# Performance work log

Measured on AMD Instinct MI355X. Metric: run time of the kernel, lower is better.

## Reference

```python
import jax, jax.numpy as jnp
import numpy as np

NEG_SLOPE = 0.2  # PyG GATConv default leaky_relu slope


def _gat_layer(x, src, dst, W, a_src, a_dst, b, N, concat):
    # x: [N, F_in]; W: [F_in, H*C]; a_src/a_dst: [H, C]; b: [H*C] or [C]
    H, C = a_src.shape
    h = (x @ W).reshape(N, H, C)                      # [N, H, C]
    al_s = jnp.einsum('nhc,hc->nh', h, a_src)          # [N, H]
    al_d = jnp.einsum('nhc,hc->nh', h, a_dst)          # [N, H]
    e = jax.nn.leaky_relu(al_s[src] + al_d[dst], NEG_SLOPE)  # [E, H]
    # segment softmax over incoming edges of each dst node
    m = jax.ops.segment_max(e, dst, num_segments=N)    # [N, H]
    ex = jnp.exp(e - m[dst])                           # [E, H]
    denom = jax.ops.segment_sum(ex, dst, num_segments=N)
    attn = ex / denom[dst]                             # [E, H]
    msg = (h[src] * attn[:, :, None]).reshape(-1, H * C)  # [E, H*C]
    out = jax.ops.segment_sum(msg, dst, num_segments=N)   # [N, H*C]
    if concat:
        return out + b
    return out.reshape(N, H, C).mean(axis=1) + b


def setup_inputs() -> dict:
    key = jax.random.key(0)
    ks = jax.random.split(key, 20)
    N, E, D, C, H = 20000, 160000, 768, 128, 4
    HC = H * C  # 512
    def glorot(k, shape):
        fan = shape[0] + shape[-1]
        return jax.random.uniform(k, shape, jnp.float32, -1.0, 1.0) * np.sqrt(6.0 / fan)
    inp = {
        'x': jax.random.normal(ks[0], (N, D), jnp.float32),
        'edge_index': jax.random.randint(ks[1], (2, E), 0, N, jnp.int64),
        'W1': glorot(ks[2], (D, HC)),  'as1': glorot(ks[3], (H, C)), 'ad1': glorot(ks[4], (H, C)), 'b1': jnp.zeros((HC,), jnp.float32),
        'W2': glorot(ks[5], (HC, HC)), 'as2': glorot(ks[6], (H, C)), 'ad2': glorot(ks[7], (H, C)), 'b2': jnp.zeros((HC,), jnp.float32),
        'W3': glorot(ks[8], (HC, C)),  'as3': glorot(ks[9], (1, C)), 'ad3': glorot(ks[10], (1, C)), 'b3': jnp.zeros((C,), jnp.float32),
        'Ws1': glorot(ks[11], (C, C // 2)), 'bs1': jnp.zeros((C // 2,), jnp.float32),
        'Ws2': glorot(ks[12], (C // 2, 1)), 'bs2': jnp.zeros((1,), jnp.float32),
    }
    return inp


def reference(x, edge_index, W1, as1, ad1, b1, W2, as2, ad2, b2, W3, as3, ad3, b3, Ws1, bs1, Ws2, bs2):
    N = x.shape[0]
    loops = jnp.arange(N, dtype=edge_index.dtype)
    src = jnp.concatenate([edge_index[0], loops])  # add self-loops (PyG default)
    dst = jnp.concatenate([edge_index[1], loops])
    h = _gat_layer(x, src, dst, W1, as1, ad1, b1, N, concat=True)
    h = jax.nn.relu(h)  # dropout is identity in eval mode
    h = _gat_layer(h, src, dst, W2, as2, ad2, b2, N, concat=True)
    h = jax.nn.relu(h)
    h = _gat_layer(h, src, dst, W3, as3, ad3, b3, N, concat=False)
    # risk scoring head: Linear -> ReLU -> Linear -> Sigmoid
    s = jax.nn.relu(h @ Ws1 + bs1)
    return jax.nn.sigmoid(s @ Ws2 + bs2)  # [N, 1]
```

## Files before the change

### kernel.cpp

```cpp
#include <hip/hip_runtime.h>
#include <hip/hip_bf16.h>
#include <math.h>

#define NEG_SLOPE 0.2f
#define MAXDEG 64

typedef __attribute__((ext_vector_type(8))) __bf16 bf16x8;
typedef __attribute__((ext_vector_type(4))) float f32x4;

__device__ inline float lrelu(float v) { return v > 0.f ? v : NEG_SLOPE * v; }

__device__ inline unsigned short f2bf(float f) {
    __hip_bfloat16 h = __float2bfloat16(f);
    return *reinterpret_cast<unsigned short*>(&h);
}
__device__ inline float bf_lo(unsigned u) { return __uint_as_float(u << 16); }
__device__ inline float bf_hi(unsigned u) { return __uint_as_float(u & 0xffff0000u); }

__device__ inline void gld16(const unsigned short* gp, unsigned short* lp) {
    __builtin_amdgcn_global_load_lds(
        (const __attribute__((address_space(1))) void*)gp,
        (__attribute__((address_space(3))) void*)lp, 16, 0, 0);
}

__device__ inline void transpose_one(const float* __restrict__ in,
                                     unsigned short* __restrict__ out,
                                     int K, int N, int idx) {
    if (idx >= K * N) return;
    int n = idx / K, k = idx % K;
    out[(size_t)n * K + k] = f2bf(in[(size_t)k * N + n]);
}

#define BARRIER()    asm volatile("s_barrier" ::: "memory")
#define WAIT_LGKM0() asm volatile("s_waitcnt lgkmcnt(0)" ::: "memory")
#define WAIT_VM0()   asm volatile("s_waitcnt vmcnt(0)" ::: "memory")
#define WAIT_VM3()   asm volatile("s_waitcnt vmcnt(3)" ::: "memory")
#define WAIT_VM6()   asm volatile("s_waitcnt vmcnt(6)" ::: "memory")

__global__ __launch_bounds__(256) void preproc_kernel(
    const float* __restrict__ x, unsigned short* __restrict__ xbf, int n4,
    const float* __restrict__ W1, unsigned short* __restrict__ W1t,
    const float* __restrict__ W2, unsigned short* __restrict__ W2t,
    const float* __restrict__ W3, unsigned short* __restrict__ W3t,
    const float* __restrict__ Ws1, unsigned short* __restrict__ Ws1t,
    const int* __restrict__ ei, int E, int N,
    int* __restrict__ cursor, int* __restrict__ csr,
    int c0, int c1, int c2, int c3, int c4,
    int D, int HC, int C) {
    int b = blockIdx.x;
    int t = threadIdx.x;
    if (b < c0) {
        int i = b * 256 + t;
        if (i < n4) {
            float4 v = reinterpret_cast<const float4*>(x)[i];
            ushort4 o;
            o.x = f2bf(v.x); o.y = f2bf(v.y); o.z = f2bf(v.z); o.w = f2bf(v.w);
            reinterpret_cast<ushort4*>(xbf)[i] = o;
        }
        return;
    }
    b -= c0;
    if (b < c1) { transpose_one(W1, W1t, D, HC, b * 256 + t); return; }
    b -= c1;
    if (b < c2) { transpose_one(W2, W2t, HC, HC, b * 256 + t); return; }
    b -= c2;
    if (b < c3) { transpose_one(W3, W3t, HC, C, b * 256 + t); return; }
    b -= c3;
    if (b < c4) { transpose_one(Ws1, Ws1t, 128, 64, b * 256 + t); return; }
    b -= c4;
    {
        int e = b * 256 + t;
        if (e < E + N) {
            int src, dst;
            if (e < E) { src = ei[e]; dst = ei[E + e]; }
            else       { src = dst = e - E; }
            int pos = atomicAdd(&cursor[dst], 1);
            if (pos < MAXDEG) csr[dst * MAXDEG + pos] = src;
        }
    }
}

template <int HEADS>
__global__ __launch_bounds__(512) void gemm_big(const unsigned short* __restrict__ A,
                                                const unsigned short* __restrict__ Bt,
                                                unsigned short* __restrict__ Cc,
                                                int M, int N, int K, int rowTiles,
                                                const float* __restrict__ a_src,
                                                const float* __restrict__ a_dst,
                                                float* __restrict__ alS,
                                                float* __restrict__ alD) {
    __shared__ unsigned short Asl[3][128 * 32];
    __shared__ unsigned short Bsl[3][256 * 32];
    const int tid  = threadIdx.x;
    const int lane = tid & 63;
    const int wave = tid >> 6;

    int r, c;
    {
        int b = blockIdx.x;
        int mainRows = rowTiles & ~7;
        int mainBlocks = mainRows * 2;
        if (b < mainBlocks) {
            int xcd = b & 7;
            c = (b >> 3) & 1;
            r = (b >> 4) * 8 + xcd;
        } else {
            int idx = b - mainBlocks;
            r = mainRows + (idx >> 1);
            c = idx & 1;
        }
    }
    const int rowBase = r * 128;
    const int colBase = c * 256;
    const int wm = (wave & 1) * 64;
    const int wn = (wave >> 1) * 64;
    const int q   = lane >> 4;
    const int l16 = lane & 15;

    const int ar  = tid >> 2;
    const int acg = (tid & 3) ^ ((ar >> 1) & 3);
    int gaA = rowBase + ar; if (gaA >= M) gaA = M - 1;
    const unsigned short* gpA0 = A + (size_t)gaA * K + acg * 8;

    const int br0  = tid >> 2;
    const int bcg0 = (tid & 3) ^ ((br0 >> 1) & 3);
    const int br1  = (tid + 512) >> 2;
    const int bcg1 = (tid & 3) ^ ((br1 >> 1) & 3);
    const unsigned short* gpB0 = Bt + (size_t)(colBase + br0) * K + bcg0 * 8;
    const unsigned short* gpB1 = Bt + (size_t)(colBase + br1) * K + bcg1 * 8;

    const int nk = K >> 5;
    f32x4 acc[4][4] = {};

    auto stage = [&](int kt, int buf) {
        gld16(gpA0 + kt * 32, &Asl[buf][tid * 8]);
        gld16(gpB0 + kt * 32, &Bsl[buf][tid * 8]);
        gld16(gpB1 + kt * 32, &Bsl[buf][(size_t)(tid + 512) * 8]);
    };
    auto compute = [&](int buf) {
        bf16x8 af[4], bfv[4];
#pragma unroll
        for (int mi = 0; mi < 4; mi++) {
            int row = wm + mi * 16 + l16;
            int ch = q ^ ((row >> 1) & 3);
            af[mi] = *reinterpret_cast<const bf16x8*>(&Asl[buf][row * 32 + ch * 8]);
        }
#pragma unroll
        for (int ni = 0; ni < 4; ni++) {
            int row = wn + ni * 16 + l16;
            int ch = q ^ ((row >> 1) & 3);
            bfv[ni] = *reinterpret_cast<const bf16x8*>(&Bsl[buf][row * 32 + ch * 8]);
        }
#pragma unroll
        for (int mi = 0; mi < 4; mi++)
#pragma unroll
            for (int ni = 0; ni < 4; ni++)
                acc[mi][ni] = __builtin_amdgcn_mfma_f32_16x16x32_bf16(af[mi], bfv[ni], acc[mi][ni], 0, 0, 0);
    };

    stage(0, 0);
    stage(1, 1);
    int buf = 0;
    for (int kt = 0; kt < nk; kt++) {
        if (kt + 2 < nk) {
            int nbuf = buf + 2; if (nbuf >= 3) nbuf -= 3;
            stage(kt + 2, nbuf);
            WAIT_VM6();
        } else if (kt + 1 < nk) {
            WAIT_VM3();
        } else {
            WAIT_VM0();
        }
        BARRIER();
        compute(buf);
        WAIT_LGKM0();
        BARRIER();
        buf++; if (buf >= 3) buf = 0;
    }

    const int headBase = colBase >> 7;
    const int hl   = wn >> 7;
    const int half = (wn >> 6) & 1;
    const float* aslp = a_src + (headBase + hl) * 128;
    const float* adlp = a_dst + (headBase + hl) * 128;
    float acoef[4], dcoef[4];
#pragma unroll
    for (int ni = 0; ni < 4; ni++) {
        int cl = half * 64 + ni * 16 + l16;
        acoef[ni] = aslp[cl];
        dcoef[ni] = adlp[cl];
    }

    float2* red = reinterpret_cast<float2*>(&Asl[0][0]);

#pragma unroll
    for (int mi = 0; mi < 4; mi++) {
#pragma unroll
        for (int rr = 0; rr < 4; rr++) {
            int lrow = wm + mi * 16 + q * 4 + rr;
            int grow = rowBase + lrow;
            bool ok = grow < M;
            float vs = 0.f, vd = 0.f;
#pragma unroll
            for (int ni = 0; ni < 4; ni++) {
                float hv = acc[mi][ni][rr];
                vs += hv * acoef[ni];
                vd += hv * dcoef[ni];
                if (ok) {
                    int gcol = colBase + wn + ni * 16 + l16;
                    Cc[(size_t)grow * N + gcol] = f2bf(hv);
                }
            }
#pragma unroll
            for (int d = 1; d < 16; d <<= 1) {
                vs += __shfl_xor(vs, d);
                vd += __shfl_xor(vd, d);
            }
            if (l16 == 0) red[lrow * 4 + hl * 2 + half] = make_float2(vs, vd);
        }
    }
    __syncthreads();
    if (tid < 256) {
        int row = tid >> 1, hh = tid & 1;
        int grow = rowBase + row;
        if (grow < M) {
            float2 a = red[row * 4 + hh * 2 + 0];
            float2 b = red[row * 4 + hh * 2 + 1];
            alS[(size_t)grow * HEADS + headBase + hh] = a.x + b.x;
            alD[(size_t)grow * HEADS + headBase + hh] = a.y + b.y;
        }
    }
}

__global__ __launch_bounds__(256) void gemm_l3(const unsigned short* __restrict__ A,
                                               const unsigned short* __restrict__ Bt,
                                               unsigned short* __restrict__ Cc,
                                               int M, int K,
                                               const float* __restrict__ a_src,
                                               const float* __restrict__ a_dst,
                                               float* __restrict__ alS,
                                               float* __restrict__ alD) {
    const int N = 128;
    __shared__ unsigned short Asl[3][64 * 32];
    __shared__ unsigned short Bsl[3][128 * 32];
    const int tid  = threadIdx.x;
    const int lane = tid & 63;
    const int wave = tid >> 6;
    const int rowBase = blockIdx.x * 64;
    const int wm = (wave & 1) * 32;
    const int wn = (wave >> 1) * 64;
    const int q   = lane >> 4;
    const int l16 = lane & 15;

    const int ar  = tid >> 2;
    const int acg = (tid & 3) ^ ((ar >> 1) & 3);
    int gaA = rowBase + ar; if (gaA >= M) gaA = M - 1;
    const unsigned short* gpA0 = A + (size_t)gaA * K + acg * 8;

    const int br0  = tid >> 2;
    const int bcg0 = (tid & 3) ^ ((br0 >> 1) & 3);
    const int br1  = (tid + 256) >> 2;
    const int bcg1 = (tid & 3) ^ ((br1 >> 1) & 3);
    const unsigned short* gpB0 = Bt + (size_t)br0 * K + bcg0 * 8;
    const unsigned short* gpB1 = Bt + (size_t)br1 * K + bcg1 * 8;

    const int nk = K >> 5;
    f32x4 acc[2][4] = {};

    auto stage = [&](int kt, int buf) {
        gld16(gpA0 + kt * 32, &Asl[buf][tid * 8]);
        gld16(gpB0 + kt * 32, &Bsl[buf][tid * 8]);
        gld16(gpB1 + kt * 32, &Bsl[buf][(size_t)(tid + 256) * 8]);
    };
    auto compute = [&](int buf) {
        bf16x8 af[2], bfv[4];
#pragma unroll
        for (int mi = 0; mi < 2; mi++) {
            int row = wm + mi * 16 + l16;
            int ch = q ^ ((row >> 1) & 3);
            af[mi] = *reinterpret_cast<const bf16x8*>(&Asl[buf][row * 32 + ch * 8]);
        }
#pragma unroll
        for (int ni = 0; ni < 4; ni++) {
            int row = wn + ni * 16 + l16;
            int ch = q ^ ((row >> 1) & 3);
            bfv[ni] = *reinterpret_cast<const bf16x8*>(&Bsl[buf][row * 32 + ch * 8]);
        }
#pragma unroll
        for (int mi = 0; mi < 2; mi++)
#pragma unroll
            for (int ni = 0; ni < 4; ni++)
                acc[mi][ni] = __builtin_amdgcn_mfma_f32_16x16x32_bf16(af[mi], bfv[ni], acc[mi][ni], 0, 0, 0);
    };

    stage(0, 0);
    stage(1, 1);
    int buf = 0;
    for (int kt = 0; kt < nk; kt++) {
        if (kt + 2 < nk) {
            int nbuf = buf + 2; if (nbuf >= 3) nbuf -= 3;
            stage(kt + 2, nbuf);
            WAIT_VM6();
        } else if (kt + 1 < nk) {
            WAIT_VM3();
        } else {
            WAIT_VM0();
        }
        BARRIER();
        compute(buf);
        WAIT_LGKM0();
        BARRIER();
        buf++; if (buf >= 3) buf = 0;
    }

    const int half = wn >> 6;
    float acoef[4], dcoef[4];
#pragma unroll
    for (int ni = 0; ni < 4; ni++) {
        int cl = wn + ni * 16 + l16;
        acoef[ni] = a_src[cl];
        dcoef[ni] = a_dst[cl];
    }

    float2* red = reinterpret_cast<float2*>(&Asl[0][0]);

#pragma unroll
    for (int mi = 0; mi < 2; mi++) {
#pragma unroll
        for (int rr = 0; rr < 4; rr++) {
            int lrow = wm + mi * 16 + q * 4 + rr;
            int grow = rowBase + lrow;
            bool ok = grow < M;
            float vs = 0.f, vd = 0.f;
#pragma unroll
            for (int ni = 0; ni < 4; ni++) {
                float hv = acc[mi][ni][rr];
                vs += hv * acoef[ni];
                vd += hv * dcoef[ni];
                if (ok) {
                    int gcol = wn + ni * 16 + l16;
                    Cc[(size_t)grow * N + gcol] = f2bf(hv);
                }
            }
#pragma unroll
            for (int d = 1; d < 16; d <<= 1) {
                vs += __shfl_xor(vs, d);
                vd += __shfl_xor(vd, d);
            }
            if (l16 == 0) red[lrow * 2 + half] = make_float2(vs, vd);
        }
    }
    __syncthreads();
    if (tid < 64) {
        int grow = rowBase + tid;
        if (grow < M) {
            float2 a = red[tid * 2 + 0];
            float2 b = red[tid * 2 + 1];
            alS[grow] = a.x + b.x;
            alD[grow] = a.y + b.y;
        }
    }
}

template <int H, int C, int MODE>
__global__ __launch_bounds__(256) void gat_aggregate(const unsigned short* __restrict__ hb,
                                                     const float* __restrict__ alS,
                                                     const float* __restrict__ alD,
                                                     const int* __restrict__ cursor,
                                                     const int* __restrict__ csr_src,
                                                     const float* __restrict__ bias,
                                                     unsigned short* __restrict__ outbuf,
                                                     int N,
                                                     const unsigned short* __restrict__ Ws1t,
                                                     const float* __restrict__ bs1,
                                                     const float* __restrict__ Ws2,
                                                     const float* __restrict__ bs2,
                                                     float* __restrict__ out) {
    constexpr int HC = H * C;
    constexpr int PER = HC / 64;
    __shared__ float hrow[4][128];

    int n = (blockIdx.x * blockDim.x + threadIdx.x) >> 6;
    int lane = threadIdx.x & 63;
    int wave = threadIdx.x >> 6;
    if (n >= N) return;
    const int* rowp = csr_src + (size_t)n * MAXDEG;

    const int grp  = lane >> 4;
    const int slot = lane & 15;
    const int gbase = lane & 48;
    const int myh  = (H == 4) ? grp : 0;
    const unsigned short* hbl = hb + (size_t)lane * PER;

    int total = cursor[n];
    const float adh = alD[n * H + myh];
    if (total > MAXDEG) total = MAXDEG;

    float m = -1e30f, dn = 0.f;
    float acc0 = 0.f, acc1 = 0.f, acc2 = 0.f, acc3 = 0.f,
          acc4 = 0.f, acc5 = 0.f, acc6 = 0.f, acc7 = 0.f;

    for (int base = 0; base < total; base += 16) {
        int cnt = total - base; if (cnt > 16) cnt = 16;
        int cntR = (cnt + 3) & ~3;
        bool act = slot < cnt;

        int s_raw = rowp[base + slot];
        int s_safe = ((unsigned)s_raw < (unsigned)N) ? s_raw : 0;
        float av = alS[(size_t)s_safe * H + myh];

        uint4 g0 = {}, g1 = {}, g2 = {}, g3 = {};
        uint4 g4 = {}, g5 = {}, g6 = {}, g7 = {};
        uint4 g8 = {}, g9 = {}, g10 = {}, g11 = {};
        uint4 g12 = {}, g13 = {}, g14 = {}, g15 = {};
        unsigned h0 = 0, h1 = 0, h2 = 0, h3 = 0;
        unsigned h4 = 0, h5 = 0, h6 = 0, h7 = 0;
        unsigned h8 = 0, h9 = 0, h10 = 0, h11 = 0;
        unsigned h12 = 0, h13 = 0, h14 = 0, h15 = 0;
#define LOADQ(GI, HI, J)                                                       \
        { int ix = __shfl(s_safe, J);                                          \
          if (PER == 8) GI = *reinterpret_cast<const uint4*>(hbl + (size_t)ix * HC); \
          else          HI = *reinterpret_cast<const unsigned*>(hbl + (size_t)ix * HC); }
        LOADQ(g0, h0, 0) LOADQ(g1, h1, 1) LOADQ(g2, h2, 2) LOADQ(g3, h3, 3)
        if (cntR > 4)  { LOADQ(g4, h4, 4)   LOADQ(g5, h5, 5)   LOADQ(g6, h6, 6)   LOADQ(g7, h7, 7) }
        if (cntR > 8)  { LOADQ(g8, h8, 8)   LOADQ(g9, h9, 9)   LOADQ(g10, h10, 10) LOADQ(g11, h11, 11) }
        if (cntR > 12) { LOADQ(g12, h12, 12) LOADQ(g13, h13, 13) LOADQ(g14, h14, 14) LOADQ(g15, h15, 15) }
#undef LOADQ

        float v = act ? lrelu(av + adh) : -1e30f;
        float mc = v;
#pragma unroll
        for (int d = 1; d < 16; d <<= 1) mc = fmaxf(mc, __shfl_xor(mc, d));
        float pl = __expf(v - mc);
        float dc = pl;
#pragma unroll
        for (int d = 1; d < 16; d <<= 1) dc += __shfl_xor(dc, d);
        float nm = fmaxf(m, mc);
        float so = __expf(m - nm);
        float sc = __expf(mc - nm);
        dn = dn * so + dc * sc;
        m = nm;
        float wl = pl * sc;

        acc0 *= so; acc1 *= so;
        if (PER == 8) {
            acc2 *= so; acc3 *= so; acc4 *= so; acc5 *= so;
            acc6 *= so; acc7 *= so;
        }

        if (PER == 8) {
#define CONSUME(G, J)                                                   \
            { uint4 rc = G; float w = __shfl(wl, gbase | J);            \
              acc0 += bf_lo(rc.x) * w; acc1 += bf_hi(rc.x) * w;         \
              acc2 += bf_lo(rc.y) * w; acc3 += bf_hi(rc.y) * w;         \
              acc4 += bf_lo(rc.z) * w; acc5 += bf_hi(rc.z) * w;         \
              acc6 += bf_lo(rc.w) * w; acc7 += bf_hi(rc.w) * w; }
            CONSUME(g0, 0) CONSUME(g1, 1) CONSUME(g2, 2) CONSUME(g3, 3)
            if (cntR > 4)  { CONSUME(g4, 4)   CONSUME(g5, 5)   CONSUME(g6, 6)   CONSUME(g7, 7) }
            if (cntR > 8)  { CONSUME(g8, 8)   CONSUME(g9, 9)   CONSUME(g10, 10) CONSUME(g11, 11) }
            if (cntR > 12) { CONSUME(g12, 12) CONSUME(g13, 13) CONSUME(g14, 14) CONSUME(g15, 15) }
#undef CONSUME
        } else {
#define CONSUME(HV, J)                                                  \
            { unsigned rc = HV; float w = __shfl(wl, gbase | J);        \
              acc0 += bf_lo(rc) * w; acc1 += bf_hi(rc) * w; }
            CONSUME(h0, 0) CONSUME(h1, 1) CONSUME(h2, 2) CONSUME(h3, 3)
            if (cntR > 4)  { CONSUME(h4, 4)   CONSUME(h5, 5)   CONSUME(h6, 6)   CONSUME(h7, 7) }
            if (cntR > 8)  { CONSUME(h8, 8)   CONSUME(h9, 9)   CONSUME(h10, 10) CONSUME(h11, 11) }
            if (cntR > 12) { CONSUME(h12, 12) CONSUME(h13, 13) CONSUME(h14, 14) CONSUME(h15, 15) }
#undef CONSUME
        }
    }

    float invd = 1.f / dn;
    const float* bp = bias + lane * PER;
    if (MODE == 0) {
        unsigned short* op = outbuf + (size_t)n * HC + lane * PER;
        float o0 = acc0 * invd + bp[0], o1 = acc1 * invd + bp[1];
        float o2 = acc2 * invd + bp[2], o3 = acc3 * invd + bp[3];
        float o4 = acc4 * invd + bp[4], o5 = acc5 * invd + bp[5];
        float o6 = acc6 * invd + bp[6], o7 = acc7 * invd + bp[7];
        o0 = fmaxf(o0, 0.f); o1 = fmaxf(o1, 0.f); o2 = fmaxf(o2, 0.f); o3 = fmaxf(o3, 0.f);
        o4 = fmaxf(o4, 0.f); o5 = fmaxf(o5, 0.f); o6 = fmaxf(o6, 0.f); o7 = fmaxf(o7, 0.f);
        op[0] = f2bf(o0); op[1] = f2bf(o1); op[2] = f2bf(o2); op[3] = f2bf(o3);
        op[4] = f2bf(o4); op[5] = f2bf(o5); op[6] = f2bf(o6); op[7] = f2bf(o7);
    } else {
        float o0 = acc0 * invd + bp[0], o1 = acc1 * invd + bp[1];
        reinterpret_cast<float2*>(&hrow[wave][0])[lane] = make_float2(o0, o1);
        WAIT_LGKM0();
        const float* hr = &hrow[wave][0];
        const unsigned short* wrow = Ws1t + (size_t)lane * 128;
        float s = bs1[lane];
#pragma unroll
        for (int k = 0; k < 128; k += 8) {
            uint4 wv = *reinterpret_cast<const uint4*>(&wrow[k]);
            s += hr[k + 0] * bf_lo(wv.x) + hr[k + 1] * bf_hi(wv.x)
               + hr[k + 2] * bf_lo(wv.y) + hr[k + 3] * bf_hi(wv.y)
               + hr[k + 4] * bf_lo(wv.z) + hr[k + 5] * bf_hi(wv.z)
               + hr[k + 6] * bf_lo(wv.w) + hr[k + 7] * bf_hi(wv.w);
        }
        float p = fmaxf(s, 0.f) * Ws2[lane];
#pragma unroll
        for (int d = 1; d < 64; d <<= 1) p += __shfl_xor(p, d);
        if (lane == 0) out[n] = 1.f / (1.f + __expf(-(p + bs2[0])));
    }
}

extern "C" void kernel_launch(void* const* d_in, const int* in_sizes, int n_in,
                              void* d_out, int out_size, void* d_ws, size_t ws_size,
                              hipStream_t stream) {
    const float* x   = (const float*)d_in[0];
    const int*   ei  = (const int*)d_in[1];
    const float* W1  = (const float*)d_in[2];
    const float* as1 = (const float*)d_in[3];
    const float* ad1 = (const float*)d_in[4];
    const float* b1  = (const float*)d_in[5];
    const float* W2  = (const float*)d_in[6];
    const float* as2 = (const float*)d_in[7];
    const float* ad2 = (const float*)d_in[8];
    const float* b2  = (const float*)d_in[9];
    const float* W3  = (const float*)d_in[10];
    const float* as3 = (const float*)d_in[11];
    const float* ad3 = (const float*)d_in[12];
    const float* b3  = (const float*)d_in[13];
    const float* Ws1 = (const float*)d_in[14];
    const float* bs1 = (const float*)d_in[15];
    const float* Ws2 = (const float*)d_in[16];
    const float* bs2 = (const float*)d_in[17];

    const int N = out_size;
    const int E = in_sizes[1] / 2;
    const int D = in_sizes[0] / N;
    const int HC = 512, H = 4, C = 128;
    const int Etot = E + N;

    char* p = (char*)d_ws;
    auto alloc = [&](size_t bytes) -> void* {
        void* q = (void*)p;
        p += (bytes + 255) & ~(size_t)255;
        return q;
    };
    char*  zbeg   = p;
    int*   cursor = (int*)alloc((size_t)N * 4);
    char*  zend   = p;
    float* alS1   = (float*)alloc((size_t)N * H * 4);
    float* alD1   = (float*)alloc((size_t)N * H * 4);
    float* alS2   = (float*)alloc((size_t)N * H * 4);
    float* alD2   = (float*)alloc((size_t)N * H * 4);
    float* alS3   = (float*)alloc((size_t)N * 4);
    float* alD3   = (float*)alloc((size_t)N * 4);
    int*   csr    = (int*)alloc((size_t)N * MAXDEG * 4);
    unsigned short* hbuf = (unsigned short*)alloc((size_t)N * HC * 2);
    unsigned short* obf  = (unsigned short*)alloc((size_t)N * HC * 2);
    unsigned short* xbf  = (unsigned short*)alloc((size_t)N * D * 2);
    unsigned short* W1t  = (unsigned short*)alloc((size_t)D * HC * 2);
    unsigned short* W2t  = (unsigned short*)alloc((size_t)HC * HC * 2);
    unsigned short* W3t  = (unsigned short*)alloc((size_t)HC * C * 2);
    unsigned short* Ws1t = (unsigned short*)alloc((size_t)C * 64 * 2);

    hipMemsetAsync(zbeg, 0, (size_t)(zend - zbeg), stream);

    {
        int n4 = N * D / 4;
        int c0 = (n4 + 255) / 256;
        int c1 = (D * HC + 255) / 256;
        int c2 = (HC * HC + 255) / 256;
        int c3 = (HC * C + 255) / 256;
        int c4 = (128 * 64 + 255) / 256;
        int c5 = (Etot + 255) / 256;
        int total = c0 + c1 + c2 + c3 + c4 + c5;
        preproc_kernel<<<total, 256, 0, stream>>>(
            x, xbf, n4, W1, W1t, W2, W2t, W3, W3t, Ws1, Ws1t,
            ei, E, N, cursor, csr, c0, c1, c2, c3, c4, D, HC, C);
    }

    int node_blocks = (N + 3) / 4;
    int rowTiles128 = (N + 127) / 128;
    int rowTiles64  = (N + 63) / 64;

    gemm_big<4><<<rowTiles128 * 2, 512, 0, stream>>>(
        xbf, W1t, hbuf, N, HC, D, rowTiles128, as1, ad1, alS1, alD1);
    gat_aggregate<4, 128, 0><<<node_blocks, 256, 0, stream>>>(
        hbuf, alS1, alD1, cursor, csr, b1, obf, N,
        nullptr, nullptr, nullptr, nullptr, nullptr);

    gemm_big<4><<<rowTiles128 * 2, 512, 0, stream>>>(
        obf, W2t, hbuf, N, HC, HC, rowTiles128, as2, ad2, alS2, alD2);
    gat_aggregate<4, 128, 0><<<node_blocks, 256, 0, stream>>>(
        hbuf, alS2, alD2, cursor, csr, b2, obf, N,
        nullptr, nullptr, nullptr, nullptr, nullptr);

    gemm_l3<<<rowTiles64, 256, 0, stream>>>(
        obf, W3t, hbuf, N, HC, as3, ad3, alS3, alD3);
    gat_aggregate<1, 128, 2><<<node_blocks, 256, 0, stream>>>(
        hbuf, alS3, alD3, cursor, csr, b3, nullptr, N,
        Ws1t, bs1, Ws2, bs2, (float*)d_out);
}
```

Before: 314.7 us.

## Stage edge indices and weights in LDS and software-pipeline neighbor gathers

The aggregate kernel now computes attention scores first, writes each chunk's source indices and softmax weights to shared memory, and then gathers neighbor feature rows four at a time with a double-buffered prefetch loop. This replaces issuing all 16 gathers up front plus per-edge shuffles. The aim is lower register pressure and fewer shuffles while keeping loads in flight. The trade-off is that fewer gathers are outstanding at once, since only 4-8 are in flight versus 16 before. It also relies on implicit wave-level LDS ordering with no barrier, and padded slots read stale sIdx entries, which are valid indices with zero-or-tiny weights.

Result: no change. 316.4 us (+0.5%).

```diff
diff --git a/kernel.cpp b/kernel.cpp
--- a/kernel.cpp
+++ b/kernel.cpp
@@ -378,23 +378,23 @@
                                                      float* __restrict__ out) {
     constexpr int HC = H * C;
     constexpr int PER = HC / 64;
+    __shared__ int   sIdx[4][16];
+    __shared__ float sW[4][64];
     __shared__ float hrow[4][128];
 
     int n = (blockIdx.x * blockDim.x + threadIdx.x) >> 6;
     int lane = threadIdx.x & 63;
     int wave = threadIdx.x >> 6;
     if (n >= N) return;
+    int total = cursor[n]; if (total > MAXDEG) total = MAXDEG;
     const int* rowp = csr_src + (size_t)n * MAXDEG;
 
     const int grp  = lane >> 4;
     const int slot = lane & 15;
-    const int gbase = lane & 48;
     const int myh  = (H == 4) ? grp : 0;
+    const float adh = alD[n * H + myh];
     const unsigned short* hbl = hb + (size_t)lane * PER;
-
-    int total = cursor[n];
-    const float adh = alD[n * H + myh];
-    if (total > MAXDEG) total = MAXDEG;
+    const float* sWrow = &sW[wave][grp * 16];
 
     float m = -1e30f, dn = 0.f;
     float acc0 = 0.f, acc1 = 0.f, acc2 = 0.f, acc3 = 0.f,
@@ -402,32 +402,10 @@
 
     for (int base = 0; base < total; base += 16) {
         int cnt = total - base; if (cnt > 16) cnt = 16;
-        int cntR = (cnt + 3) & ~3;
         bool act = slot < cnt;
-
-        int s_raw = rowp[base + slot];
-        int s_safe = ((unsigned)s_raw < (unsigned)N) ? s_raw : 0;
-        float av = alS[(size_t)s_safe * H + myh];
-
-        uint4 g0 = {}, g1 = {}, g2 = {}, g3 = {};
-        uint4 g4 = {}, g5 = {}, g6 = {}, g7 = {};
-        uint4 g8 = {}, g9 = {}, g10 = {}, g11 = {};
-        uint4 g12 = {}, g13 = {}, g14 = {}, g15 = {};
-        unsigned h0 = 0, h1 = 0, h2 = 0, h3 = 0;
-        unsigned h4 = 0, h5 = 0, h6 = 0, h7 = 0;
-        unsigned h8 = 0, h9 = 0, h10 = 0, h11 = 0;
-        unsigned h12 = 0, h13 = 0, h14 = 0, h15 = 0;
-#define LOADQ(GI, HI, J)                                                       \
-        { int ix = __shfl(s_safe, J);                                          \
-          if (PER == 8) GI = *reinterpret_cast<const uint4*>(hbl + (size_t)ix * HC); \
-          else          HI = *reinterpret_cast<const unsigned*>(hbl + (size_t)ix * HC); }
-        LOADQ(g0, h0, 0) LOADQ(g1, h1, 1) LOADQ(g2, h2, 2) LOADQ(g3, h3, 3)
-        if (cntR > 4)  { LOADQ(g4, h4, 4)   LOADQ(g5, h5, 5)   LOADQ(g6, h6, 6)   LOADQ(g7, h7, 7) }
-        if (cntR > 8)  { LOADQ(g8, h8, 8)   LOADQ(g9, h9, 9)   LOADQ(g10, h10, 10) LOADQ(g11, h11, 11) }
-        if (cntR > 12) { LOADQ(g12, h12, 12) LOADQ(g13, h13, 13) LOADQ(g14, h14, 14) LOADQ(g15, h15, 15) }
-#undef LOADQ
-
-        float v = act ? lrelu(av + adh) : -1e30f;
+        int s_l = rowp[act ? (base + slot) : base];
+        float v = act ? lrelu(alS[s_l * H + myh] + adh) : -1e30f;
+
         float mc = v;
 #pragma unroll
         for (int d = 1; d < 16; d <<= 1) mc = fmaxf(mc, __shfl_xor(mc, d));
@@ -442,33 +420,72 @@
         m = nm;
         float wl = pl * sc;
 
+        if (lane < 16) sIdx[wave][lane] = s_l;
+        sW[wave][lane] = wl;
+
         acc0 *= so; acc1 *= so;
         if (PER == 8) {
             acc2 *= so; acc3 *= so; acc4 *= so; acc5 *= so;
             acc6 *= so; acc7 *= so;
         }
 
+        int cntR = (cnt + 3) & ~3;
+
         if (PER == 8) {
-#define CONSUME(G, J)                                                   \
-            { uint4 rc = G; float w = __shfl(wl, gbase | J);            \
-              acc0 += bf_lo(rc.x) * w; acc1 += bf_hi(rc.x) * w;         \
-              acc2 += bf_lo(rc.y) * w; acc3 += bf_hi(rc.y) * w;         \
-              acc4 += bf_lo(rc.z) * w; acc5 += bf_hi(rc.z) * w;         \
-              acc6 += bf_lo(rc.w) * w; acc7 += bf_hi(rc.w) * w; }
-            CONSUME(g0, 0) CONSUME(g1, 1) CONSUME(g2, 2) CONSUME(g3, 3)
-            if (cntR > 4)  { CONSUME(g4, 4)   CONSUME(g5, 5)   CONSUME(g6, 6)   CONSUME(g7, 7) }
-            if (cntR > 8)  { CONSUME(g8, 8)   CONSUME(g9, 9)   CONSUME(g10, 10) CONSUME(g11, 11) }
-            if (cntR > 12) { CONSUME(g12, 12) CONSUME(g13, 13) CONSUME(g14, 14) CONSUME(g15, 15) }
+            int4   sI = *reinterpret_cast<const int4*>(&sIdx[wave][0]);
+            float4 wv = *reinterpret_cast<const float4*>(&sWrow[0]);
+            uint4 gA0 = *reinterpret_cast<const uint4*>(hbl + (size_t)sI.x * HC);
+            uint4 gA1 = *reinterpret_cast<const uint4*>(hbl + (size_t)sI.y * HC);
+            uint4 gA2 = *reinterpret_cast<const uint4*>(hbl + (size_t)sI.z * HC);
+            uint4 gA3 = *reinterpret_cast<const uint4*>(hbl + (size_t)sI.w * HC);
+            for (int i = 0; i < cntR; i += 4) {
+                int4 sI2 = {}; float4 wv2 = {};
+                uint4 gB0 = {}, gB1 = {}, gB2 = {}, gB3 = {};
+                if (i + 4 < cntR) {
+                    sI2 = *reinterpret_cast<const int4*>(&sIdx[wave][i + 4]);
+                    wv2 = *reinterpret_cast<const float4*>(&sWrow[i + 4]);
+                    gB0 = *reinterpret_cast<const uint4*>(hbl + (size_t)sI2.x * HC);
+                    gB1 = *reinterpret_cast<const uint4*>(hbl + (size_t)sI2.y * HC);
+                    gB2 = *reinterpret_cast<const uint4*>(hbl + (size_t)sI2.z * HC);
+                    gB3 = *reinterpret_cast<const uint4*>(hbl + (size_t)sI2.w * HC);
+                }
+#define CONSUME(G, W)                                                   \
+                { uint4 rc = G; float w = W;                            \
+                  acc0 += bf_lo(rc.x) * w; acc1 += bf_hi(rc.x) * w;     \
+                  acc2 += bf_lo(rc.y) * w; acc3 += bf_hi(rc.y) * w;     \
+                  acc4 += bf_lo(rc.z) * w; acc5 += bf_hi(rc.z) * w;     \
+                  acc6 += bf_lo(rc.w) * w; acc7 += bf_hi(rc.w) * w; }
+                CONSUME(gA0, wv.x); CONSUME(gA1, wv.y);
+                CONSUME(gA2, wv.z); CONSUME(gA3, wv.w);
 #undef CONSUME
+                sI = sI2; wv = wv2;
+                gA0 = gB0; gA1 = gB1; gA2 = gB2; gA3 = gB3;
+            }
         } else {
-#define CONSUME(HV, J)                                                  \
-            { unsigned rc = HV; float w = __shfl(wl, gbase | J);        \
-              acc0 += bf_lo(rc) * w; acc1 += bf_hi(rc) * w; }
-            CONSUME(h0, 0) CONSUME(h1, 1) CONSUME(h2, 2) CONSUME(h3, 3)
-            if (cntR > 4)  { CONSUME(h4, 4)   CONSUME(h5, 5)   CONSUME(h6, 6)   CONSUME(h7, 7) }
-            if (cntR > 8)  { CONSUME(h8, 8)   CONSUME(h9, 9)   CONSUME(h10, 10) CONSUME(h11, 11) }
-            if (cntR > 12) { CONSUME(h12, 12) CONSUME(h13, 13) CONSUME(h14, 14) CONSUME(h15, 15) }
-#undef CONSUME
+            int4   sI = *reinterpret_cast<const int4*>(&sIdx[wave][0]);
+            float4 wv = *reinterpret_cast<const float4*>(&sWrow[0]);
+            unsigned gA0 = *reinterpret_cast<const unsigned*>(hbl + (size_t)sI.x * HC);
+            unsigned gA1 = *reinterpret_cast<const unsigned*>(hbl + (size_t)sI.y * HC);
+            unsigned gA2 = *reinterpret_cast<const unsigned*>(hbl + (size_t)sI.z * HC);
+            unsigned gA3 = *reinterpret_cast<const unsigned*>(hbl + (size_t)sI.w * HC);
+            for (int i = 0; i < cntR; i += 4) {
+                int4 sI2 = {}; float4 wv2 = {};
+                unsigned gB0 = 0, gB1 = 0, gB2 = 0, gB3 = 0;
+                if (i + 4 < cntR) {
+                    sI2 = *reinterpret_cast<const int4*>(&sIdx[wave][i + 4]);
+                    wv2 = *reinterpret_cast<const float4*>(&sWrow[i + 4]);
+                    gB0 = *reinterpret_cast<const unsigned*>(hbl + (size_t)sI2.x * HC);
+                    gB1 = *reinterpret_cast<const unsigned*>(hbl + (size_t)sI2.y * HC);
+                    gB2 = *reinterpret_cast<const unsigned*>(hbl + (size_t)sI2.z * HC);
+                    gB3 = *reinterpret_cast<const unsigned*>(hbl + (size_t)sI2.w * HC);
+                }
+                acc0 += bf_lo(gA0) * wv.x; acc1 += bf_hi(gA0) * wv.x;
+                acc0 += bf_lo(gA1) * wv.y; acc1 += bf_hi(gA1) * wv.y;
+                acc0 += bf_lo(gA2) * wv.z; acc1 += bf_hi(gA2) * wv.z;
+                acc0 += bf_lo(gA3) * wv.w; acc1 += bf_hi(gA3) * wv.w;
+                sI = sI2; wv = wv2;
+                gA0 = gB0; gA1 = gB1; gA2 = gB2; gA3 = gB3;
+            }
         }
     }
 
```
